# Kernel tuning notes

Hardware: AMD Instinct MI355X
Metric: run time of the kernel (lower is better)

Reference implementation:

```python
import jax, jax.numpy as jnp
import numpy as np

N = 50000      # nodes
E = 1600000    # edges (avg degree 32)
IN, HID, OUT = 32, 32, 10
K = 2          # kernel_size (dim=1, degree=1 open B-spline -> basis (1-u, u))


def setup_inputs() -> dict:
    key = jax.random.key(0)
    ks = jax.random.split(key, 10)
    x = jax.random.normal(ks[0], (N, IN), dtype=jnp.float32)
    edge_index = jax.random.randint(ks[1], (2, E), 0, N, dtype=jnp.int64)
    edge_attr = jax.random.uniform(ks[2], (E, 1), dtype=jnp.float32)  # pseudo-coords in [0,1)
    s1 = 1.0 / np.sqrt(IN * K)
    s2 = 1.0 / np.sqrt(HID * K)
    W1 = jax.random.uniform(ks[3], (K, IN, HID), minval=-s1, maxval=s1, dtype=jnp.float32)
    root1 = jax.random.uniform(ks[4], (IN, HID), minval=-s1, maxval=s1, dtype=jnp.float32)
    b1 = jnp.zeros((HID,), jnp.float32)
    W2 = jax.random.uniform(ks[5], (K, HID, OUT), minval=-s2, maxval=s2, dtype=jnp.float32)
    root2 = jax.random.uniform(ks[6], (HID, OUT), minval=-s2, maxval=s2, dtype=jnp.float32)
    b2 = jnp.zeros((OUT,), jnp.float32)
    return {"x": x, "edge_index": edge_index, "edge_attr": edge_attr,
            "W1": W1, "root1": root1, "b1": b1,
            "W2": W2, "root2": root2, "b2": b2}


def spline_conv(x, edge_index, edge_attr, W, W_root, b):
    # SplineConv, dim=1, kernel_size=2, degree=1, aggr='mean', root_weight, bias.
    # Basis for pseudo u in [0,1): B_0(u) = 1-u, B_1(u) = u.
    src, dst = edge_index[0], edge_index[1]
    u = edge_attr[:, 0]                      # [E]
    h0 = x @ W[0]                            # [N, out] node-level transform, then gather
    h1 = x @ W[1]
    msg = (1.0 - u)[:, None] * h0[src] + u[:, None] * h1[src]   # [E, out]
    n = x.shape[0]
    agg = jax.ops.segment_sum(msg, dst, num_segments=n)
    deg = jax.ops.segment_sum(jnp.ones((src.shape[0],), x.dtype), dst, num_segments=n)
    mean = agg / jnp.maximum(deg, 1.0)[:, None]
    return mean + x @ W_root + b


def reference(x, edge_index, edge_attr, W1, root1, b1, W2, root2, b2):
    # Dropout is identity in eval mode.
    h = jax.nn.relu(spline_conv(x, edge_index, edge_attr, W1, root1, b1))
    h = spline_conv(h, edge_index, edge_attr, W2, root2, b2)
    return jax.nn.log_softmax(h, axis=1)
```

## Files before the change

### kernel.cpp

```cpp
#include <hip/hip_runtime.h>
#include <math.h>

#define GSHIFT 7
#define GSIZE  128
#define NBSZ   512
#define EPB    2048
#define CAP    5120

#define UDEC1 0.00390625f
#define UDEC2 0.001953125f

__device__ __forceinline__ unsigned bf16rn(float f) {
    unsigned u = __float_as_uint(f);
    return (u + 0x7FFFu + ((u >> 16) & 1u)) >> 16;
}
__device__ __forceinline__ float bfl(unsigned v) { return __uint_as_float(v << 16); }
__device__ __forceinline__ float bfh(unsigned v) { return __uint_as_float(v & 0xFFFF0000u); }

__global__ __launch_bounds__(256) void k_prep(const float* __restrict__ x,
                                              unsigned* __restrict__ x_pk,
                                              int* __restrict__ bcount,
                                              int n, int NB) {
    int t = blockIdx.x * 256 + threadIdx.x;
    if (t < NB) bcount[t] = 0;
    if (t >= n) return;
    const float4* xp = (const float4*)(x + (size_t)t * 32);
    #pragma unroll
    for (int k = 0; k < 4; k++) {
        float4 a = xp[2 * k], c = xp[2 * k + 1];
        uint4 pk;
        pk.x = bf16rn(a.x) | (bf16rn(a.y) << 16);
        pk.y = bf16rn(a.z) | (bf16rn(a.w) << 16);
        pk.z = bf16rn(c.x) | (bf16rn(c.y) << 16);
        pk.w = bf16rn(c.z) | (bf16rn(c.w) << 16);
        *(uint4*)(x_pk + (size_t)t * 16 + k * 4) = pk;
    }
}

__global__ __launch_bounds__(512) void k_part(const int* __restrict__ src,
                                              const int* __restrict__ dst,
                                              const float* __restrict__ attr,
                                              int* __restrict__ bcount,
                                              unsigned* __restrict__ su,
                                              int E_, int NB) {
    __shared__ int lh[NBSZ];
    __shared__ int lst[NBSZ];
    __shared__ int lcur[NBSZ];
    __shared__ int gbase[NBSZ];
    __shared__ int wsum[8];
    __shared__ unsigned srt[EPB];
    __shared__ unsigned short lbk[EPB];
    int tid = threadIdx.x, lane = tid & 63, w = tid >> 6;
    lh[tid] = 0;
    __syncthreads();
    int base = blockIdx.x * EPB;
    int d[4];
    unsigned rec[4];
    #pragma unroll
    for (int k = 0; k < 4; k++) {
        int e = base + k * 512 + tid;
        bool val = e < E_;
        int dd = val ? dst[e] : 0;
        int s  = val ? src[e] : 0;
        float a = val ? attr[e] : 0.f;
        d[k] = val ? (dd >> GSHIFT) : -1;
        unsigned uq = (unsigned)(a * 256.0f);
        rec[k] = (unsigned)(s & 0xFFFF) | ((unsigned)(dd & (GSIZE - 1)) << 16) | (uq << 24);
        if (d[k] >= 0) atomicAdd(&lh[d[k]], 1);
    }
    __syncthreads();
    int v = lh[tid];
    int incl = v;
    #pragma unroll
    for (int o = 1; o < 64; o <<= 1) {
        int t2 = __shfl_up(incl, o);
        if (lane >= o) incl += t2;
    }
    if (lane == 63) wsum[w] = incl;
    __syncthreads();
    int woff = 0;
    for (int k = 0; k < w; k++) woff += wsum[k];
    int excl = woff + incl - v;
    lst[tid] = excl;
    lcur[tid] = excl;
    if (tid < NB) gbase[tid] = atomicAdd(&bcount[tid], v);
    __syncthreads();
    #pragma unroll
    for (int k = 0; k < 4; k++) {
        if (d[k] >= 0) {
            int pos = atomicAdd(&lcur[d[k]], 1);
            srt[pos] = rec[k];
            lbk[pos] = (unsigned short)d[k];
        }
    }
    __syncthreads();
    int total = E_ - base; if (total > EPB) total = EPB;
    for (int p = tid; p < total; p += 512) {
        int b = lbk[p];
        su[(size_t)b * CAP + gbase[b] + (p - lst[b])] = srt[p];
    }
}

__global__ __launch_bounds__(1024) void k_sort(const int* __restrict__ bcount,
                                               const unsigned* __restrict__ su,
                                               unsigned* __restrict__ su2,
                                               int* __restrict__ rowptr,
                                               int* __restrict__ deg, int n) {
    __shared__ int hist[GSIZE];
    __shared__ int cur[GSIZE];
    __shared__ int wsum2[2];
    __shared__ int stot;
    __shared__ unsigned sorted[CAP];
    int b = blockIdx.x, tid = threadIdx.x;
    size_t basee = (size_t)b * CAP;
    int cnt = bcount[b];
    if (tid < GSIZE) hist[tid] = 0;
    __syncthreads();
    for (int e = tid; e < cnt; e += 1024)
        atomicAdd(&hist[(su[basee + e] >> 16) & (GSIZE - 1)], 1);
    __syncthreads();
    int lane = tid & 63, w = tid >> 6;
    int v = 0, pv = 0, incl = 0;
    if (tid < GSIZE) {
        v = hist[tid];
        pv = (v + 3) & ~3;
        incl = pv;
        #pragma unroll
        for (int o = 1; o < 64; o <<= 1) {
            int t2 = __shfl_up(incl, o);
            if (lane >= o) incl += t2;
        }
        if (lane == 63) wsum2[w] = incl;
    }
    __syncthreads();
    if (tid < GSIZE) {
        int woff = (w == 1) ? wsum2[0] : 0;
        int excl = woff + incl - pv;
        cur[tid] = excl;
        if (tid == GSIZE - 1) stot = excl + pv;
        int node = (b << GSHIFT) + tid;
        if (node < n) { rowptr[node] = (int)basee + excl; deg[node] = v; }
        for (int p = excl + v; p < excl + pv; p++) sorted[p] = 0;
    }
    __syncthreads();
    for (int e = tid; e < cnt; e += 1024) {
        unsigned r = su[basee + e];
        int pos = atomicAdd(&cur[(r >> 16) & (GSIZE - 1)], 1);
        sorted[pos] = r;
    }
    __syncthreads();
    int tot4 = stot >> 2;
    uint4* dp = (uint4*)(su2 + basee);
    for (int p = tid; p < tot4; p += 1024)
        dp[p] = *(const uint4*)(sorted + p * 4);
}

__global__ __launch_bounds__(256) void k_agg1s(const int* __restrict__ rowptr,
                                               const int* __restrict__ deg,
                                               const unsigned* __restrict__ su2,
                                               const unsigned* __restrict__ x_pk,
                                               unsigned* __restrict__ sums, int n) {
    int lane = threadIdx.x & 63;
    int node = (blockIdx.x * 4 + (threadIdx.x >> 6)) * 4 + (lane >> 4);
    int qt = (lane >> 2) & 3;
    int q  = lane & 3;
    if (node >= n) return;
    int start = rowptr[node], dgi = deg[node], end = start + dgi;
    int q4 = (dgi + 3) >> 2;
    int qb = q4 >> 2, rem = q4 & 3;
    int myq = qb + (qt < rem ? 1 : 0);
    int e0 = start + (qt * qb + min(qt, rem)) * 4;
    float a0[8] = {0,0,0,0,0,0,0,0}, a1[8] = {0,0,0,0,0,0,0,0};
    for (int i = 0; i < myq; i++) {
        int e = e0 + i * 4;
        uint4 rq = *(const uint4*)(su2 + e);
        unsigned rr[4] = {rq.x, rq.y, rq.z, rq.w};
        #pragma unroll
        for (int k = 0; k < 4; k++) {
            bool v = (e + k) < end;
            unsigned r = rr[k];
            uint4 g = *(const uint4*)(x_pk + (size_t)(r & 0xFFFFu) * 16 + q * 4);
            float wv = v ? 1.f : 0.f;
            float u = v ? fmaf((float)(r >> 24), UDEC1, UDEC2) : 0.f;
            unsigned gw[4] = {g.x, g.y, g.z, g.w};
            #pragma unroll
            for (int m2 = 0; m2 < 4; m2++) {
                float fl = bfl(gw[m2]), fh = bfh(gw[m2]);
                a0[2*m2]   = fmaf(wv, fl, a0[2*m2]);
                a0[2*m2+1] = fmaf(wv, fh, a0[2*m2+1]);
                a1[2*m2]   = fmaf(u, fl, a1[2*m2]);
                a1[2*m2+1] = fmaf(u, fh, a1[2*m2+1]);
            }
        }
    }
    #pragma unroll
    for (int k = 0; k < 8; k++) {
        a0[k] += __shfl_xor(a0[k], 4); a1[k] += __shfl_xor(a1[k], 4);
        a0[k] += __shfl_xor(a0[k], 8); a1[k] += __shfl_xor(a1[k], 8);
    }
    if (qt == 0) {
        uint4 p0, p1;
        p0.x = bf16rn(a0[0]) | (bf16rn(a1[0]) << 16);
        p0.y = bf16rn(a0[1]) | (bf16rn(a1[1]) << 16);
        p0.z = bf16rn(a0[2]) | (bf16rn(a1[2]) << 16);
        p0.w = bf16rn(a0[3]) | (bf16rn(a1[3]) << 16);
        p1.x = bf16rn(a0[4]) | (bf16rn(a1[4]) << 16);
        p1.y = bf16rn(a0[5]) | (bf16rn(a1[5]) << 16);
        p1.z = bf16rn(a0[6]) | (bf16rn(a1[6]) << 16);
        p1.w = bf16rn(a0[7]) | (bf16rn(a1[7]) << 16);
        *(uint4*)(sums + (size_t)node * 32 + q * 8)     = p0;
        *(uint4*)(sums + (size_t)node * 32 + q * 8 + 4) = p1;
    }
}

__global__ __launch_bounds__(256, 1) void k_mid(const float* __restrict__ x,
                                                const unsigned* __restrict__ sums,
                                                const int* __restrict__ deg,
                                                const float* __restrict__ W1,
                                                const float* __restrict__ root1,
                                                const float* __restrict__ b1,
                                                const float* __restrict__ W2,
                                                const float* __restrict__ root2,
                                                unsigned* __restrict__ gg,
                                                float* __restrict__ hr, int n) {
    __shared__ float sW0[1024], sDl[1024], sRt[1024];
    __shared__ float sA0[320], sD2[320], sR2[320];
    __shared__ float sB1[32];
    int tid = threadIdx.x;
    for (int i = tid; i < 1024; i += 256) {
        float w0 = W1[i];
        sW0[i] = w0; sDl[i] = W1[1024 + i] - w0; sRt[i] = root1[i];
    }
    for (int i = tid; i < 320; i += 256) {
        float a0 = W2[i];
        sA0[i] = a0; sD2[i] = W2[320 + i] - a0; sR2[i] = root2[i];
    }
    if (tid < 32) sB1[tid] = b1[tid];
    __syncthreads();
    int node = blockIdx.x * 256 + tid;
    if (node >= n) return;
    float invd = 1.0f / fmaxf((float)deg[node], 1.0f);
    float s0[32], s1[32], xv[32];
    const uint4* sp = (const uint4*)(sums + (size_t)node * 32);
    #pragma unroll
    for (int k = 0; k < 8; k++) {
        uint4 t = sp[k];
        unsigned a[4] = {t.x, t.y, t.z, t.w};
        #pragma unroll
        for (int j = 0; j < 4; j++) {
            s0[4 * k + j] = bfl(a[j]) * invd;
            s1[4 * k + j] = bfh(a[j]) * invd;
        }
    }
    const float4* xp = (const float4*)(x + (size_t)node * 32);
    #pragma unroll
    for (int k = 0; k < 8; k++) {
        float4 t = xp[k];
        xv[4*k] = t.x; xv[4*k+1] = t.y; xv[4*k+2] = t.z; xv[4*k+3] = t.w;
    }
    float h[32];
    #pragma unroll
    for (int c = 0; c < 32; c++) h[c] = sB1[c];
    for (int i = 0; i < 32; i++) {
        float si0 = s0[i], si1 = s1[i], xi = xv[i];
        #pragma unroll
        for (int cq = 0; cq < 8; cq++) {
            float4 w0 = *(const float4*)(sW0 + i * 32 + cq * 4);
            float4 dl = *(const float4*)(sDl + i * 32 + cq * 4);
            float4 rt = *(const float4*)(sRt + i * 32 + cq * 4);
            h[cq*4+0] = fmaf(si0, w0.x, fmaf(si1, dl.x, fmaf(xi, rt.x, h[cq*4+0])));
            h[cq*4+1] = fmaf(si0, w0.y, fmaf(si1, dl.y, fmaf(xi, rt.y, h[cq*4+1])));
            h[cq*4+2] = fmaf(si0, w0.z, fmaf(si1, dl.z, fmaf(xi, rt.z, h[cq*4+2])));
            h[cq*4+3] = fmaf(si0, w0.w, fmaf(si1, dl.w, fmaf(xi, rt.w, h[cq*4+3])));
        }
    }
    #pragma unroll
    for (int c = 0; c < 32; c++) h[c] = fmaxf(h[c], 0.f);
    float g0a[10], gda[10], gra[10];
    #pragma unroll
    for (int c = 0; c < 10; c++) { g0a[c] = 0.f; gda[c] = 0.f; gra[c] = 0.f; }
    for (int i = 0; i < 32; i++) {
        float hi = h[i];
        #pragma unroll
        for (int c2 = 0; c2 < 5; c2++) {
            float2 wa = *(const float2*)(sA0 + i * 10 + c2 * 2);
            float2 wd = *(const float2*)(sD2 + i * 10 + c2 * 2);
            float2 wr = *(const float2*)(sR2 + i * 10 + c2 * 2);
            g0a[c2*2+0] = fmaf(hi, wa.x, g0a[c2*2+0]);
            g0a[c2*2+1] = fmaf(hi, wa.y, g0a[c2*2+1]);
            gda[c2*2+0] = fmaf(hi, wd.x, gda[c2*2+0]);
            gda[c2*2+1] = fmaf(hi, wd.y, gda[c2*2+1]);
            gra[c2*2+0] = fmaf(hi, wr.x, gra[c2*2+0]);
            gra[c2*2+1] = fmaf(hi, wr.y, gra[c2*2+1]);
        }
    }
    unsigned pk[16];
    #pragma unroll
    for (int c = 0; c < 10; c++) pk[c] = bf16rn(g0a[c]) | (bf16rn(gda[c]) << 16);
    #pragma unroll
    for (int c = 10; c < 16; c++) pk[c] = 0;
    #pragma unroll
    for (int c = 0; c < 16; c += 4)
        *(uint4*)(gg + (size_t)node * 16 + c) =
            make_uint4(pk[c], pk[c+1], pk[c+2], pk[c+3]);
    #pragma unroll
    for (int c = 0; c < 10; c += 2)
        *(float2*)(hr + (size_t)node * 10 + c) = make_float2(gra[c], gra[c+1]);
}

__global__ __launch_bounds__(256) void k_agg2(const int* __restrict__ rowptr,
                                              const int* __restrict__ deg,
                                              const unsigned* __restrict__ su2,
                                              const unsigned* __restrict__ gg,
                                              const float* __restrict__ hr,
                                              const float* __restrict__ b2,
                                              float* __restrict__ out, int n) {
    int lane = threadIdx.x & 63;
    int node = (blockIdx.x * 4 + (threadIdx.x >> 6)) * 4 + (lane >> 4);
    int qt = (lane >> 2) & 3;
    int q  = lane & 3;
    if (node >= n) return;
    int start = rowptr[node], dgi = deg[node], end = start + dgi;
    int q4 = (dgi + 3) >> 2;
    int qb = q4 >> 2, rem = q4 & 3;
    int myq = qb + (qt < rem ? 1 : 0);
    int e0 = start + (qt * qb + min(qt, rem)) * 4;
    float acc[4] = {0, 0, 0, 0};
    for (int i = 0; i < myq; i++) {
        int e = e0 + i * 4;
        uint4 rq = *(const uint4*)(su2 + e);
        unsigned rr[4] = {rq.x, rq.y, rq.z, rq.w};
        #pragma unroll
        for (int k = 0; k < 4; k++) {
            bool v = (e + k) < end;
            unsigned r = rr[k];
            uint4 g = *(const uint4*)(gg + (size_t)(r & 0xFFFFu) * 16 + q * 4);
            float wv = v ? 1.f : 0.f;
            float u = v ? fmaf((float)(r >> 24), UDEC1, UDEC2) : 0.f;
            acc[0] = fmaf(wv, bfl(g.x), fmaf(u, bfh(g.x), acc[0]));
            acc[1] = fmaf(wv, bfl(g.y), fmaf(u, bfh(g.y), acc[1]));
            acc[2] = fmaf(wv, bfl(g.z), fmaf(u, bfh(g.z), acc[2]));
            acc[3] = fmaf(wv, bfl(g.w), fmaf(u, bfh(g.w), acc[3]));
        }
    }
    #pragma unroll
    for (int k = 0; k < 4; k++) {
        acc[k] += __shfl_xor(acc[k], 4);
        acc[k] += __shfl_xor(acc[k], 8);
    }
    float invd = 1.0f / fmaxf((float)dgi, 1.0f);
    int c0 = q * 4;
    float lg[4];
    float m = -INFINITY;
    #pragma unroll
    for (int k = 0; k < 4; k++) {
        int c = c0 + k;
        if (c < 10) {
            lg[k] = fmaf(acc[k], invd, hr[(size_t)node * 10 + c] + b2[c]);
            m = fmaxf(m, lg[k]);
        } else lg[k] = -INFINITY;
    }
    m = fmaxf(m, __shfl_xor(m, 1));
    m = fmaxf(m, __shfl_xor(m, 2));
    float ex = 0.f;
    #pragma unroll
    for (int k = 0; k < 4; k++)
        if (c0 + k < 10) ex += __expf(lg[k] - m);
    ex += __shfl_xor(ex, 1);
    ex += __shfl_xor(ex, 2);
    float lse = m + __logf(ex);
    if (qt == 0 && c0 < 10) {
        *(float2*)(out + (size_t)node * 10 + c0) =
            make_float2(lg[0] - lse, lg[1] - lse);
        if (c0 + 2 < 10)
            *(float2*)(out + (size_t)node * 10 + c0 + 2) =
                make_float2(lg[2] - lse, lg[3] - lse);
    }
}

extern "C" void kernel_launch(void* const* d_in, const int* in_sizes, int n_in,
                              void* d_out, int out_size, void* d_ws, size_t ws_size,
                              hipStream_t stream) {
    const float* x     = (const float*)d_in[0];
    const int*   ei    = (const int*)d_in[1];
    const float* attr  = (const float*)d_in[2];
    const float* W1    = (const float*)d_in[3];
    const float* root1 = (const float*)d_in[4];
    const float* b1    = (const float*)d_in[5];
    const float* W2    = (const float*)d_in[6];
    const float* root2 = (const float*)d_in[7];
    const float* b2    = (const float*)d_in[8];
    float* out = (float*)d_out;

    int N_ = in_sizes[0] / 32;
    int E_ = in_sizes[1] / 2;
    const int* src = ei;
    const int* dst = ei + E_;
    int NB = (N_ + GSIZE - 1) >> GSHIFT;
    int NP = (E_ + EPB - 1) / EPB;

    char* ws = (char*)d_ws;
    size_t off = 0;
    auto alloc = [&](size_t bytes) -> void* {
        void* p = ws + off;
        off += (bytes + 255) & ~(size_t)255;
        return p;
    };
    int*      bcount = (int*)     alloc((size_t)NB * 4);
    unsigned* su     = (unsigned*)alloc(((size_t)NB * CAP + 64) * 4);
    unsigned* su2    = (unsigned*)alloc(((size_t)NB * CAP + 64) * 4);
    int*      rowptr = (int*)     alloc((size_t)N_ * 4);
    int*      deg    = (int*)     alloc((size_t)N_ * 4);
    unsigned* x_pk   = (unsigned*)alloc((size_t)N_ * 16 * 4);
    unsigned* sums   = (unsigned*)alloc((size_t)N_ * 32 * 4);
    unsigned* gg     = (unsigned*)alloc((size_t)N_ * 16 * 4);
    float*    hr     = (float*)   alloc((size_t)N_ * 10 * 4);

    int prep_blocks = (N_ > NB ? N_ : NB);
    k_prep <<<(prep_blocks + 255) / 256, 256, 0, stream>>>(x, x_pk, bcount, N_, NB);
    k_part <<<NP, 512, 0, stream>>>(src, dst, attr, bcount, su, E_, NB);
    k_sort <<<NB, 1024, 0, stream>>>(bcount, su, su2, rowptr, deg, N_);
    k_agg1s<<<(N_ + 15) / 16, 256, 0, stream>>>(rowptr, deg, su2, x_pk, sums, N_);
    k_mid  <<<(N_ + 255) / 256, 256, 0, stream>>>(x, sums, deg, W1, root1, b1,
                                                  W2, root2, gg, hr, N_);
    k_agg2 <<<(N_ + 15) / 16, 256, 0, stream>>>(rowptr, deg, su2, gg, hr, b2, out, N_);
}
```

Before: 90.19 us.

## Fuse bucket sort, layer-1 aggregation and node MLP into one per-bucket kernel

Shrinks destination buckets to 64 nodes and merges the sort, first-layer gather/aggregation and dense node transform into a single kernel. Each block aggregates from the bucket's sorted edges in shared memory and runs the layer-1/layer-2 weight products on shared-memory tiles. This removes the global `sums` intermediate, its write and read-back, and two kernel launches. The partition kernel is widened to 1024 threads and 4096 edges per block to match. In exchange, each node now gets 8 lanes for its gather instead of 16, and the larger shared-memory footprint lowers occupancy.

```diff
diff --git a/kernel.cpp b/kernel.cpp
--- a/kernel.cpp
+++ b/kernel.cpp
@@ -1,11 +1,11 @@
 #include <hip/hip_runtime.h>
 #include <math.h>
 
-#define GSHIFT 7
-#define GSIZE  128
-#define NBSZ   512
-#define EPB    2048
-#define CAP    5120
+#define GSHIFT 6
+#define GSIZE  64
+#define NBSZ   1024
+#define EPB    4096
+#define CAP    3072
 
 #define UDEC1 0.00390625f
 #define UDEC2 0.001953125f
@@ -37,18 +37,18 @@
     }
 }
 
-__global__ __launch_bounds__(512) void k_part(const int* __restrict__ src,
-                                              const int* __restrict__ dst,
-                                              const float* __restrict__ attr,
-                                              int* __restrict__ bcount,
-                                              unsigned* __restrict__ su,
-                                              int E_, int NB) {
+__global__ __launch_bounds__(1024) void k_part(const int* __restrict__ src,
+                                               const int* __restrict__ dst,
+                                               const float* __restrict__ attr,
+                                               int* __restrict__ bcount,
+                                               unsigned* __restrict__ su,
+                                               int E_, int NB) {
     __shared__ int lh[NBSZ];
     __shared__ int lst[NBSZ];
     __shared__ int lcur[NBSZ];
     __shared__ int gbase[NBSZ];
-    __shared__ int wsum[8];
-    __shared__ unsigned srt[EPB];
+    __shared__ int wsum[16];
+    __shared__ __align__(16) unsigned srt[EPB];
     __shared__ unsigned short lbk[EPB];
     int tid = threadIdx.x, lane = tid & 63, w = tid >> 6;
     lh[tid] = 0;
@@ -58,7 +58,7 @@
     unsigned rec[4];
     #pragma unroll
     for (int k = 0; k < 4; k++) {
-        int e = base + k * 512 + tid;
+        int e = base + k * 1024 + tid;
         bool val = e < E_;
         int dd = val ? dst[e] : 0;
         int s  = val ? src[e] : 0;
@@ -95,217 +95,185 @@
     }
     __syncthreads();
     int total = E_ - base; if (total > EPB) total = EPB;
-    for (int p = tid; p < total; p += 512) {
+    for (int p = tid; p < total; p += 1024) {
         int b = lbk[p];
         su[(size_t)b * CAP + gbase[b] + (p - lst[b])] = srt[p];
     }
 }
 
-__global__ __launch_bounds__(1024) void k_sort(const int* __restrict__ bcount,
+__global__ __launch_bounds__(512) void k_fused(const int* __restrict__ bcount,
                                                const unsigned* __restrict__ su,
                                                unsigned* __restrict__ su2,
                                                int* __restrict__ rowptr,
-                                               int* __restrict__ deg, int n) {
-    __shared__ int hist[GSIZE];
-    __shared__ int cur[GSIZE];
-    __shared__ int wsum2[2];
+                                               int* __restrict__ deg,
+                                               const unsigned* __restrict__ x_pk,
+                                               const float* __restrict__ x,
+                                               const float* __restrict__ W1,
+                                               const float* __restrict__ root1,
+                                               const float* __restrict__ b1,
+                                               const float* __restrict__ W2,
+                                               const float* __restrict__ root2,
+                                               unsigned* __restrict__ gg,
+                                               float* __restrict__ hr, int n) {
+    __shared__ __align__(16) float sW0[1024], sDl[1024], sRt[1024];
+    __shared__ float sA0[320], sD2[320], sR2[320], sB1[32];
+    __shared__ __align__(16) unsigned sorted[CAP];
+    __shared__ __align__(16) float accum[GSIZE * 64];
+    __shared__ __align__(16) float xl[GSIZE * 32];
+    __shared__ __align__(16) float hl[GSIZE * 32];
+    __shared__ int hist[GSIZE], cur[GSIZE], sstart[GSIZE], sdeg[GSIZE];
     __shared__ int stot;
-    __shared__ unsigned sorted[CAP];
+
     int b = blockIdx.x, tid = threadIdx.x;
     size_t basee = (size_t)b * CAP;
     int cnt = bcount[b];
+    int node0 = b << GSHIFT;
+
     if (tid < GSIZE) hist[tid] = 0;
-    __syncthreads();
-    for (int e = tid; e < cnt; e += 1024)
-        atomicAdd(&hist[(su[basee + e] >> 16) & (GSIZE - 1)], 1);
-    __syncthreads();
-    int lane = tid & 63, w = tid >> 6;
-    int v = 0, pv = 0, incl = 0;
-    if (tid < GSIZE) {
-        v = hist[tid];
-        pv = (v + 3) & ~3;
-        incl = pv;
+    for (int i = tid; i < 1024; i += 512) {
+        float w0 = W1[i];
+        sW0[i] = w0; sDl[i] = W1[1024 + i] - w0; sRt[i] = root1[i];
+    }
+    for (int i = tid; i < 320; i += 512) {
+        float a0 = W2[i];
+        sA0[i] = a0; sD2[i] = W2[320 + i] - a0; sR2[i] = root2[i];
+    }
+    if (tid < 32) sB1[tid] = b1[tid];
+    {
+        size_t xbase = (size_t)node0 * 32;
+        size_t xlim = (size_t)n * 32;
+        for (int i = tid; i < GSIZE * 32; i += 512)
+            xl[i] = (xbase + i < xlim) ? x[xbase + i] : 0.f;
+    }
+    __syncthreads();
+
+    for (int e = tid; e < cnt; e += 512)
+        atomicAdd(&hist[(su[basee + e] >> 16) & 63], 1);
+    __syncthreads();
+
+    if (tid < 64) {
+        int v = hist[tid];
+        int pv = (v + 3) & ~3;
+        int incl = pv;
         #pragma unroll
         for (int o = 1; o < 64; o <<= 1) {
             int t2 = __shfl_up(incl, o);
-            if (lane >= o) incl += t2;
-        }
-        if (lane == 63) wsum2[w] = incl;
-    }
-    __syncthreads();
-    if (tid < GSIZE) {
-        int woff = (w == 1) ? wsum2[0] : 0;
-        int excl = woff + incl - pv;
-        cur[tid] = excl;
-        if (tid == GSIZE - 1) stot = excl + pv;
-        int node = (b << GSHIFT) + tid;
+            if (tid >= o) incl += t2;
+        }
+        int excl = incl - pv;
+        cur[tid] = excl; sstart[tid] = excl; sdeg[tid] = v;
+        int node = node0 + tid;
         if (node < n) { rowptr[node] = (int)basee + excl; deg[node] = v; }
+        if (tid == 63) stot = excl + pv;
         for (int p = excl + v; p < excl + pv; p++) sorted[p] = 0;
     }
     __syncthreads();
-    for (int e = tid; e < cnt; e += 1024) {
+
+    for (int e = tid; e < cnt; e += 512) {
         unsigned r = su[basee + e];
-        int pos = atomicAdd(&cur[(r >> 16) & (GSIZE - 1)], 1);
+        int pos = atomicAdd(&cur[(r >> 16) & 63], 1);
         sorted[pos] = r;
     }
     __syncthreads();
-    int tot4 = stot >> 2;
-    uint4* dp = (uint4*)(su2 + basee);
-    for (int p = tid; p < tot4; p += 1024)
-        dp[p] = *(const uint4*)(sorted + p * 4);
-}
-
-__global__ __launch_bounds__(256) void k_agg1s(const int* __restrict__ rowptr,
-                                               const int* __restrict__ deg,
-                                               const unsigned* __restrict__ su2,
-                                               const unsigned* __restrict__ x_pk,
-                                               unsigned* __restrict__ sums, int n) {
-    int lane = threadIdx.x & 63;
-    int node = (blockIdx.x * 4 + (threadIdx.x >> 6)) * 4 + (lane >> 4);
-    int qt = (lane >> 2) & 3;
-    int q  = lane & 3;
-    if (node >= n) return;
-    int start = rowptr[node], dgi = deg[node], end = start + dgi;
-    int q4 = (dgi + 3) >> 2;
-    int qb = q4 >> 2, rem = q4 & 3;
-    int myq = qb + (qt < rem ? 1 : 0);
-    int e0 = start + (qt * qb + min(qt, rem)) * 4;
-    float a0[8] = {0,0,0,0,0,0,0,0}, a1[8] = {0,0,0,0,0,0,0,0};
-    for (int i = 0; i < myq; i++) {
-        int e = e0 + i * 4;
-        uint4 rq = *(const uint4*)(su2 + e);
-        unsigned rr[4] = {rq.x, rq.y, rq.z, rq.w};
+
+    {
+        int tot4 = stot >> 2;
+        uint4* dp = (uint4*)(su2 + basee);
+        for (int p = tid; p < tot4; p += 512)
+            dp[p] = *(const uint4*)(sorted + p * 4);
+    }
+    {
+        int nl = tid >> 3, q = tid & 3, half = (tid >> 2) & 1;
+        int st = sstart[nl], dgi = sdeg[nl];
+        int endl = st + dgi;
+        int q4 = (dgi + 3) >> 2;
+        int hq = q4 >> 1, rem = q4 & 1;
+        int myq = hq + (half < rem ? 1 : 0);
+        int e0 = st + (half * hq + min(half, rem)) * 4;
+        float a0[8] = {0,0,0,0,0,0,0,0}, a1[8] = {0,0,0,0,0,0,0,0};
+        for (int i = 0; i < myq; i++) {
+            int e = e0 + i * 4;
+            uint4 rq = *(const uint4*)(sorted + e);
+            unsigned rr[4] = {rq.x, rq.y, rq.z, rq.w};
+            #pragma unroll
+            for (int k = 0; k < 4; k++) {
+                bool v = (e + k) < endl;
+                unsigned r = rr[k];
+                uint4 g = *(const uint4*)(x_pk + (size_t)(r & 0xFFFFu) * 16 + q * 4);
+                float wv = v ? 1.f : 0.f;
+                float u = v ? fmaf((float)(r >> 24), UDEC1, UDEC2) : 0.f;
+                unsigned gw[4] = {g.x, g.y, g.z, g.w};
+                #pragma unroll
+                for (int m2 = 0; m2 < 4; m2++) {
+                    float fl = bfl(gw[m2]), fh = bfh(gw[m2]);
+                    a0[2*m2]   = fmaf(wv, fl, a0[2*m2]);
+                    a0[2*m2+1] = fmaf(wv, fh, a0[2*m2+1]);
+                    a1[2*m2]   = fmaf(u, fl, a1[2*m2]);
+                    a1[2*m2+1] = fmaf(u, fh, a1[2*m2+1]);
+                }
+            }
+        }
         #pragma unroll
-        for (int k = 0; k < 4; k++) {
-            bool v = (e + k) < end;
-            unsigned r = rr[k];
-            uint4 g = *(const uint4*)(x_pk + (size_t)(r & 0xFFFFu) * 16 + q * 4);
-            float wv = v ? 1.f : 0.f;
-            float u = v ? fmaf((float)(r >> 24), UDEC1, UDEC2) : 0.f;
-            unsigned gw[4] = {g.x, g.y, g.z, g.w};
+        for (int k = 0; k < 8; k++) {
+            a0[k] += __shfl_xor(a0[k], 4);
+            a1[k] += __shfl_xor(a1[k], 4);
+        }
+        if (half == 0) {
             #pragma unroll
-            for (int m2 = 0; m2 < 4; m2++) {
-                float fl = bfl(gw[m2]), fh = bfh(gw[m2]);
-                a0[2*m2]   = fmaf(wv, fl, a0[2*m2]);
-                a0[2*m2+1] = fmaf(wv, fh, a0[2*m2+1]);
-                a1[2*m2]   = fmaf(u, fl, a1[2*m2]);
-                a1[2*m2+1] = fmaf(u, fh, a1[2*m2+1]);
+            for (int k = 0; k < 8; k++) {
+                accum[nl * 64 + q * 8 + k]      = a0[k];
+                accum[nl * 64 + 32 + q * 8 + k] = a1[k];
             }
         }
     }
-    #pragma unroll
-    for (int k = 0; k < 8; k++) {
-        a0[k] += __shfl_xor(a0[k], 4); a1[k] += __shfl_xor(a1[k], 4);
-        a0[k] += __shfl_xor(a0[k], 8); a1[k] += __shfl_xor(a1[k], 8);
-    }
-    if (qt == 0) {
-        uint4 p0, p1;
-        p0.x = bf16rn(a0[0]) | (bf16rn(a1[0]) << 16);
-        p0.y = bf16rn(a0[1]) | (bf16rn(a1[1]) << 16);
-        p0.z = bf16rn(a0[2]) | (bf16rn(a1[2]) << 16);
-        p0.w = bf16rn(a0[3]) | (bf16rn(a1[3]) << 16);
-        p1.x = bf16rn(a0[4]) | (bf16rn(a1[4]) << 16);
-        p1.y = bf16rn(a0[5]) | (bf16rn(a1[5]) << 16);
-        p1.z = bf16rn(a0[6]) | (bf16rn(a1[6]) << 16);
-        p1.w = bf16rn(a0[7]) | (bf16rn(a1[7]) << 16);
-        *(uint4*)(sums + (size_t)node * 32 + q * 8)     = p0;
-        *(uint4*)(sums + (size_t)node * 32 + q * 8 + 4) = p1;
-    }
-}
-
-__global__ __launch_bounds__(256, 1) void k_mid(const float* __restrict__ x,
-                                                const unsigned* __restrict__ sums,
-                                                const int* __restrict__ deg,
-                                                const float* __restrict__ W1,
-                                                const float* __restrict__ root1,
-                                                const float* __restrict__ b1,
-                                                const float* __restrict__ W2,
-                                                const float* __restrict__ root2,
-                                                unsigned* __restrict__ gg,
-                                                float* __restrict__ hr, int n) {
-    __shared__ float sW0[1024], sDl[1024], sRt[1024];
-    __shared__ float sA0[320], sD2[320], sR2[320];
-    __shared__ float sB1[32];
-    int tid = threadIdx.x;
-    for (int i = tid; i < 1024; i += 256) {
-        float w0 = W1[i];
-        sW0[i] = w0; sDl[i] = W1[1024 + i] - w0; sRt[i] = root1[i];
-    }
-    for (int i = tid; i < 320; i += 256) {
-        float a0 = W2[i];
-        sA0[i] = a0; sD2[i] = W2[320 + i] - a0; sR2[i] = root2[i];
-    }
-    if (tid < 32) sB1[tid] = b1[tid];
-    __syncthreads();
-    int node = blockIdx.x * 256 + tid;
-    if (node >= n) return;
-    float invd = 1.0f / fmaxf((float)deg[node], 1.0f);
-    float s0[32], s1[32], xv[32];
-    const uint4* sp = (const uint4*)(sums + (size_t)node * 32);
-    #pragma unroll
-    for (int k = 0; k < 8; k++) {
-        uint4 t = sp[k];
-        unsigned a[4] = {t.x, t.y, t.z, t.w};
-        #pragma unroll
-        for (int j = 0; j < 4; j++) {
-            s0[4 * k + j] = bfl(a[j]) * invd;
-            s1[4 * k + j] = bfh(a[j]) * invd;
-        }
-    }
-    const float4* xp = (const float4*)(x + (size_t)node * 32);
-    #pragma unroll
-    for (int k = 0; k < 8; k++) {
-        float4 t = xp[k];
-        xv[4*k] = t.x; xv[4*k+1] = t.y; xv[4*k+2] = t.z; xv[4*k+3] = t.w;
-    }
-    float h[32];
-    #pragma unroll
-    for (int c = 0; c < 32; c++) h[c] = sB1[c];
-    for (int i = 0; i < 32; i++) {
-        float si0 = s0[i], si1 = s1[i], xi = xv[i];
-        #pragma unroll
-        for (int cq = 0; cq < 8; cq++) {
-            float4 w0 = *(const float4*)(sW0 + i * 32 + cq * 4);
-            float4 dl = *(const float4*)(sDl + i * 32 + cq * 4);
-            float4 rt = *(const float4*)(sRt + i * 32 + cq * 4);
-            h[cq*4+0] = fmaf(si0, w0.x, fmaf(si1, dl.x, fmaf(xi, rt.x, h[cq*4+0])));
-            h[cq*4+1] = fmaf(si0, w0.y, fmaf(si1, dl.y, fmaf(xi, rt.y, h[cq*4+1])));
-            h[cq*4+2] = fmaf(si0, w0.z, fmaf(si1, dl.z, fmaf(xi, rt.z, h[cq*4+2])));
-            h[cq*4+3] = fmaf(si0, w0.w, fmaf(si1, dl.w, fmaf(xi, rt.w, h[cq*4+3])));
-        }
-    }
-    #pragma unroll
-    for (int c = 0; c < 32; c++) h[c] = fmaxf(h[c], 0.f);
-    float g0a[10], gda[10], gra[10];
-    #pragma unroll
-    for (int c = 0; c < 10; c++) { g0a[c] = 0.f; gda[c] = 0.f; gra[c] = 0.f; }
-    for (int i = 0; i < 32; i++) {
-        float hi = h[i];
-        #pragma unroll
-        for (int c2 = 0; c2 < 5; c2++) {
-            float2 wa = *(const float2*)(sA0 + i * 10 + c2 * 2);
-            float2 wd = *(const float2*)(sD2 + i * 10 + c2 * 2);
-            float2 wr = *(const float2*)(sR2 + i * 10 + c2 * 2);
-            g0a[c2*2+0] = fmaf(hi, wa.x, g0a[c2*2+0]);
-            g0a[c2*2+1] = fmaf(hi, wa.y, g0a[c2*2+1]);
-            gda[c2*2+0] = fmaf(hi, wd.x, gda[c2*2+0]);
-            gda[c2*2+1] = fmaf(hi, wd.y, gda[c2*2+1]);
-            gra[c2*2+0] = fmaf(hi, wr.x, gra[c2*2+0]);
-            gra[c2*2+1] = fmaf(hi, wr.y, gra[c2*2+1]);
-        }
-    }
-    unsigned pk[16];
-    #pragma unroll
-    for (int c = 0; c < 10; c++) pk[c] = bf16rn(g0a[c]) | (bf16rn(gda[c]) << 16);
-    #pragma unroll
-    for (int c = 10; c < 16; c++) pk[c] = 0;
-    #pragma unroll
-    for (int c = 0; c < 16; c += 4)
-        *(uint4*)(gg + (size_t)node * 16 + c) =
-            make_uint4(pk[c], pk[c+1], pk[c+2], pk[c+3]);
-    #pragma unroll
-    for (int c = 0; c < 10; c += 2)
-        *(float2*)(hr + (size_t)node * 10 + c) = make_float2(gra[c], gra[c+1]);
+    __syncthreads();
+
+    {
+        int nl = tid >> 3, j = tid & 7;
+        float invd = 1.0f / fmaxf((float)sdeg[nl], 1.0f);
+        float4 hv = *(const float4*)(sB1 + 0);
+        hv.x = sB1[4*j]; hv.y = sB1[4*j+1]; hv.z = sB1[4*j+2]; hv.w = sB1[4*j+3];
+        for (int i = 0; i < 32; i++) {
+            float s0 = accum[nl * 64 + i] * invd;
+            float s1 = accum[nl * 64 + 32 + i] * invd;
+            float xi = xl[nl * 32 + i];
+            float4 w0 = *(const float4*)(sW0 + i * 32 + 4 * j);
+            float4 dl = *(const float4*)(sDl + i * 32 + 4 * j);
+            float4 rt = *(const float4*)(sRt + i * 32 + 4 * j);
+            hv.x = fmaf(s0, w0.x, fmaf(s1, dl.x, fmaf(xi, rt.x, hv.x)));
+            hv.y = fmaf(s0, w0.y, fmaf(s1, dl.y, fmaf(xi, rt.y, hv.y)));
+            hv.z = fmaf(s0, w0.z, fmaf(s1, dl.z, fmaf(xi, rt.z, hv.z)));
+            hv.w = fmaf(s0, w0.w, fmaf(s1, dl.w, fmaf(xi, rt.w, hv.w)));
+        }
+        hv.x = fmaxf(hv.x, 0.f); hv.y = fmaxf(hv.y, 0.f);
+        hv.z = fmaxf(hv.z, 0.f); hv.w = fmaxf(hv.w, 0.f);
+        *(float4*)(hl + nl * 32 + 4 * j) = hv;
+    }
+    __syncthreads();
+
+    {
+        int nl = tid >> 3, j = tid & 7;
+        int node = node0 + nl;
+        if (node < n) {
+            #pragma unroll
+            for (int ci = 0; ci < 2; ci++) {
+                int c = j + ci * 8;
+                if (c < 10) {
+                    float g0 = 0.f, gd = 0.f, gr = 0.f;
+                    for (int i = 0; i < 32; i++) {
+                        float hi = hl[nl * 32 + i];
+                        g0 = fmaf(hi, sA0[i * 10 + c], g0);
+                        gd = fmaf(hi, sD2[i * 10 + c], gd);
+                        gr = fmaf(hi, sR2[i * 10 + c], gr);
+                    }
+                    gg[(size_t)node * 16 + c] = bf16rn(g0) | (bf16rn(gd) << 16);
+                    hr[(size_t)node * 10 + c] = gr;
+                } else {
+                    gg[(size_t)node * 16 + c] = 0;
+                }
+            }
+        }
+    }
 }
 
 __global__ __launch_bounds__(256) void k_agg2(const int* __restrict__ rowptr,
@@ -412,16 +380,13 @@
     int*      rowptr = (int*)     alloc((size_t)N_ * 4);
     int*      deg    = (int*)     alloc((size_t)N_ * 4);
     unsigned* x_pk   = (unsigned*)alloc((size_t)N_ * 16 * 4);
-    unsigned* sums   = (unsigned*)alloc((size_t)N_ * 32 * 4);
     unsigned* gg     = (unsigned*)alloc((size_t)N_ * 16 * 4);
     float*    hr     = (float*)   alloc((size_t)N_ * 10 * 4);
 
     int prep_blocks = (N_ > NB ? N_ : NB);
     k_prep <<<(prep_blocks + 255) / 256, 256, 0, stream>>>(x, x_pk, bcount, N_, NB);
-    k_part <<<NP, 512, 0, stream>>>(src, dst, attr, bcount, su, E_, NB);
-    k_sort <<<NB, 1024, 0, stream>>>(bcount, su, su2, rowptr, deg, N_);
-    k_agg1s<<<(N_ + 15) / 16, 256, 0, stream>>>(rowptr, deg, su2, x_pk, sums, N_);
-    k_mid  <<<(N_ + 255) / 256, 256, 0, stream>>>(x, sums, deg, W1, root1, b1,
-                                                  W2, root2, gg, hr, N_);
+    k_part <<<NP, 1024, 0, stream>>>(src, dst, attr, bcount, su, E_, NB);
+    k_fused<<<NB, 512, 0, stream>>>(bcount, su, su2, rowptr, deg, x_pk, x,
+                                    W1, root1, b1, W2, root2, gg, hr, N_);
     k_agg2 <<<(N_ + 15) / 16, 256, 0, stream>>>(rowptr, deg, su2, gg, hr, b2, out, N_);
 }
```

Result: faster. 82.33 us (-8.7%).
